# Kernel tuning notes

Hardware: AMD Instinct MI355X
Metric: run time of the kernel (lower is better)

## Reference

```python
import jax, jax.numpy as jnp
import numpy as np

BN_EPS = 1e-5


def setup_inputs() -> dict:
    key = jax.random.key(0)
    ks = jax.random.split(key, 6)
    B, C, K, N = 4, 64, 16, 16384  # batch, feat channels, neighbors, points
    W_OUT = 16  # weightnet output channels (fixed by Linear(16*mlp[-1], ...))
    xyz = jax.random.normal(ks[0], (B, N, 3), dtype=jnp.float32)
    points = jax.random.normal(ks[1], (B, C, K, N), dtype=jnp.float32)
    coordinate = jax.random.normal(ks[2], (B, 3, K, N), dtype=jnp.float32)
    w1 = jax.random.normal(ks[3], (W_OUT, 3), dtype=jnp.float32) * 0.5
    b1 = jnp.zeros((W_OUT,), dtype=jnp.float32)
    lin_w = jax.random.normal(ks[4], (C, W_OUT * C), dtype=jnp.float32) * (1.0 / np.sqrt(W_OUT * C))
    lin_b = jnp.zeros((C,), dtype=jnp.float32)
    gamma = jnp.ones((C,), dtype=jnp.float32)
    beta = jnp.zeros((C,), dtype=jnp.float32)
    return {"xyz": xyz, "points": points, "coordinate": coordinate,
            "w1": w1, "b1": b1, "lin_w": lin_w, "lin_b": lin_b,
            "gamma": gamma, "beta": beta}


def reference(xyz, points, coordinate, w1, b1, lin_w, lin_b, gamma, beta):
    B, C, K, N = points.shape
    # weightnet: 1x1 conv (3 -> 16) + ReLU over coordinate [B,3,K,N] -> [B,16,K,N]
    weights = jax.nn.relu(jnp.einsum('oc,bckn->bokn', w1, coordinate) + b1[None, :, None, None])
    # per-point aggregation: [B,N,C,K] @ [B,N,K,16] -> [B,N,C,16]
    new_points = jnp.einsum('bckn,bokn->bnco', points, weights)
    new_points = new_points.reshape(B, N, C * 16)  # [B, N, 16*C]
    # linear projection 16*C -> C
    new_points = jnp.einsum('bnk,ok->bno', new_points, lin_w) + lin_b  # [B, N, C]
    # BatchNorm1d over channel dim (training-mode batch stats), layout [B, C, N]
    new_points = new_points.transpose(0, 2, 1)  # [B, C, N]
    mean = jnp.mean(new_points, axis=(0, 2), keepdims=True)
    var = jnp.var(new_points, axis=(0, 2), keepdims=True)
    new_points = (new_points - mean) * jax.lax.rsqrt(var + BN_EPS)
    new_points = new_points * gamma[None, :, None] + beta[None, :, None]
    new_points = jax.nn.relu(new_points)  # [B, C, N]
    return (xyz, new_points)
```

## Files before the change

kernel.cpp:

```cpp
#include <hip/hip_runtime.h>

#define BB 4
#define CC 64
#define KK 16
#define NN 16384
#define NT 64
#define CH 8
#define NCH 8

typedef __attribute__((ext_vector_type(8))) short short8;
typedef __attribute__((ext_vector_type(4))) float floatx4;
typedef __attribute__((ext_vector_type(2))) _Float16 half2v;

__device__ __forceinline__ unsigned short f2bf_rtne(float x) {
    unsigned u = __builtin_bit_cast(unsigned, x);
    u += 0x7FFFu + ((u >> 16) & 1u);
    return (unsigned short)(u >> 16);
}

__device__ __forceinline__ unsigned pack_bf16x2(float lo, float hi) {
    unsigned a = __builtin_bit_cast(unsigned, lo) + 0x8000u;
    unsigned b = __builtin_bit_cast(unsigned, hi) + 0x8000u;
    return __builtin_amdgcn_perm(b, a, 0x07060302u);
}

__device__ __forceinline__ half2v cvt2h(float a, float b) {
    return __builtin_bit_cast(half2v, __builtin_amdgcn_cvt_pkrtz(a, b));
}

#if __has_builtin(__builtin_amdgcn_fdot2)
#define DOT2(a, b, c) __builtin_amdgcn_fdot2((a), (b), (c), false)
#else
__device__ __forceinline__ float dot2_fb(half2v a, half2v b, float c) {
    return fmaf((float)a[0], (float)b[0], fmaf((float)a[1], (float)b[1], c));
}
#define DOT2(a, b, c) dot2_fb((a), (b), (c))
#endif

__global__ __launch_bounds__(256)
void prep_bfrag(const float* __restrict__ lin_w, unsigned short* __restrict__ bfrag)
{
    const int tid  = blockIdx.x * 256 + threadIdx.x;
    const int lane = tid & 63;
    const int g    = tid >> 6;
    const int ci   = g >> 4;
    const int kk   = (g >> 2) & 3;
    const int nt   = g & 3;
    const int r    = lane & 15;
    const int sq   = lane >> 4;

    const float* src = lin_w + (size_t)(nt * 16 + r) * 1024 + ci * 128 + kk * 32 + sq * 8;
    unsigned short v[8];
    #pragma unroll
    for (int j = 0; j < 8; ++j) v[j] = f2bf_rtne(src[j]);
    *(uint4*)(bfrag + ((size_t)g * 64 + lane) * 8) = *(const uint4*)v;
}

__global__ __launch_bounds__(256, 4)
void fused_main(const float* __restrict__ points,
                const float* __restrict__ coordinate,
                const float* __restrict__ w1,
                const float* __restrict__ b1,
                const unsigned short* __restrict__ bfrag,
                float* __restrict__ y_out)
{
    __shared__ __align__(16) unsigned short s_a[NT][136];

    const int t    = threadIdx.x;
    const int lane = t & 63;
    const int q    = __builtin_amdgcn_readfirstlane(t >> 6);
    const int r    = lane & 15;
    const int sq   = lane >> 4;

    const int bid = blockIdx.x;
    const int b   = bid >> 8;
    const int n0  = (bid & 255) * NT;

    half2v wh[4][8];
    {
        const float* coordB = coordinate + (size_t)b * 3 * KK * NN + n0 + lane;
        float c0[KK], c1[KK], c2[KK];
        #pragma unroll
        for (int k = 0; k < KK; ++k) {
            c0[k] = coordB[(0 * KK + k) * NN];
            c1[k] = coordB[(1 * KK + k) * NN];
            c2[k] = coordB[(2 * KK + k) * NN];
        }
        #pragma unroll
        for (int j = 0; j < 4; ++j) {
            const int o = 4 * q + j;
            const float w1x = w1[o * 3 + 0];
            const float w1y = w1[o * 3 + 1];
            const float w1z = w1[o * 3 + 2];
            const float bo  = b1[o];
            #pragma unroll
            for (int kp = 0; kp < 8; ++kp) {
                float v0 = fmaf(w1x, c0[2 * kp],     fmaf(w1y, c1[2 * kp],     fmaf(w1z, c2[2 * kp],     bo)));
                float v1 = fmaf(w1x, c0[2 * kp + 1], fmaf(w1y, c1[2 * kp + 1], fmaf(w1z, c2[2 * kp + 1], bo)));
                wh[j][kp] = cvt2h(fmaxf(v0, 0.0f), fmaxf(v1, 0.0f));
            }
        }
    }

    floatx4 acc[4];
    #pragma unroll
    for (int nt = 0; nt < 4; ++nt) acc[nt] = (floatx4){0.f, 0.f, 0.f, 0.f};

    const float* pB = points + (size_t)b * CC * KK * NN + n0 + lane;

    for (int ci = 0; ci < NCH; ++ci) {
        uint2 packA[CH];
        #pragma unroll
        for (int cl = 0; cl < CH; ++cl) {
            const float* pc = pB + (size_t)(ci * CH + cl) * KK * NN;
            float pv[KK];
            #pragma unroll
            for (int k = 0; k < KK; ++k) pv[k] = pc[(size_t)k * NN];
            half2v ph[8];
            #pragma unroll
            for (int kp = 0; kp < 8; ++kp)
                ph[kp] = cvt2h(pv[2 * kp], pv[2 * kp + 1]);
            float a4[4];
            #pragma unroll
            for (int j = 0; j < 4; ++j) {
                float a = 0.f;
                #pragma unroll
                for (int kp = 0; kp < 8; ++kp) a = DOT2(ph[kp], wh[j][kp], a);
                a4[j] = a;
            }
            packA[cl].x = pack_bf16x2(a4[0], a4[1]);
            packA[cl].y = pack_bf16x2(a4[2], a4[3]);
        }

        __syncthreads();
        #pragma unroll
        for (int cl = 0; cl < CH; ++cl)
            *(uint2*)&s_a[lane][cl * 16 + 4 * q] = packA[cl];
        __syncthreads();

        #pragma unroll
        for (int kk = 0; kk < 4; ++kk) {
            const short8 af = *(const short8*)&s_a[16 * q + r][kk * 32 + sq * 8];
            #pragma unroll
            for (int nt = 0; nt < 4; ++nt) {
                const short8 bf = *(const short8*)
                    (bfrag + ((((size_t)ci * 4 + kk) * 4 + nt) * 64 + lane) * 8);
                acc[nt] = __builtin_amdgcn_mfma_f32_16x16x32_bf16(af, bf, acc[nt], 0, 0, 0);
            }
        }
    }

    float* yB = y_out + (size_t)b * CC * NN + n0;
    #pragma unroll
    for (int nt = 0; nt < 4; ++nt) {
        const int oc = nt * 16 + r;
        const float4 v = make_float4(acc[nt][0], acc[nt][1], acc[nt][2], acc[nt][3]);
        *(float4*)(yB + (size_t)oc * NN + 16 * q + 4 * sq) = v;
    }
}

__global__ __launch_bounds__(256)
void bn_reduce(const float* __restrict__ y, float* __restrict__ part)
{
    const int ch = blockIdx.x & 63;
    const int b  = blockIdx.x >> 6;
    const int t  = threadIdx.x;
    const float4* p = (const float4*)(y + ((size_t)b * CC + ch) * NN);
    float s = 0.f, ss = 0.f;
    for (int i = t; i < NN / 4; i += 256) {
        const float4 v = p[i];
        s  += v.x + v.y + v.z + v.w;
        ss += v.x * v.x + v.y * v.y + v.z * v.z + v.w * v.w;
    }
    #pragma unroll
    for (int m = 1; m < 64; m <<= 1) {
        s  += __shfl_xor(s, m);
        ss += __shfl_xor(ss, m);
    }
    __shared__ float rs[4], rss[4];
    if ((t & 63) == 0) { rs[t >> 6] = s; rss[t >> 6] = ss; }
    __syncthreads();
    if (t == 0) {
        part[blockIdx.x]       = rs[0] + rs[1] + rs[2] + rs[3];
        part[256 + blockIdx.x] = rss[0] + rss[1] + rss[2] + rss[3];
    }
}

__global__ void bn_stats(const float* __restrict__ part,
                         const float* __restrict__ gamma,
                         const float* __restrict__ beta,
                         float* __restrict__ ab)
{
    const int ch = threadIdx.x;
    float S = 0.f, SS = 0.f;
    #pragma unroll
    for (int b = 0; b < BB; ++b) {
        S  += part[b * 64 + ch];
        SS += part[256 + b * 64 + ch];
    }
    const float inv  = 1.0f / (float)(BB * NN);
    const float mean = S * inv;
    const float var  = SS * inv - mean * mean;
    const float a    = gamma[ch] * rsqrtf(var + 1e-5f);
    ab[ch]      = a;
    ab[CC + ch] = beta[ch] - mean * a;
}

__global__ __launch_bounds__(256)
void bn_apply(float* __restrict__ y, const float* __restrict__ ab)
{
    const size_t i = (size_t)blockIdx.x * 256 + threadIdx.x;
    float4* p = (float4*)y;
    float4 v = p[i];
    const int ch = (int)((i * 4) >> 14) & 63;
    const float a = ab[ch], bb = ab[CC + ch];
    v.x = fmaxf(fmaf(a, v.x, bb), 0.0f);
    v.y = fmaxf(fmaf(a, v.y, bb), 0.0f);
    v.z = fmaxf(fmaf(a, v.z, bb), 0.0f);
    v.w = fmaxf(fmaf(a, v.w, bb), 0.0f);
    p[i] = v;
}

extern "C" void kernel_launch(void* const* d_in, const int* in_sizes, int n_in,
                              void* d_out, int out_size, void* d_ws, size_t ws_size,
                              hipStream_t stream)
{
    const float* xyz        = (const float*)d_in[0];
    const float* points     = (const float*)d_in[1];
    const float* coordinate = (const float*)d_in[2];
    const float* w1         = (const float*)d_in[3];
    const float* b1         = (const float*)d_in[4];
    const float* lin_w      = (const float*)d_in[5];
    const float* gamma      = (const float*)d_in[7];
    const float* beta       = (const float*)d_in[8];

    float* out = (float*)d_out;

    unsigned short* bfrag = (unsigned short*)d_ws;
    float* part = (float*)d_ws + 32768;
    float* ab   = part + 512;

    const size_t xyz_elems = (size_t)BB * NN * 3;
    (void)hipMemcpyAsync(out, xyz, xyz_elems * sizeof(float),
                         hipMemcpyDeviceToDevice, stream);

    float* y_out = out + xyz_elems;

    prep_bfrag<<<32, 256, 0, stream>>>(lin_w, bfrag);
    fused_main<<<BB * (NN / NT), 256, 0, stream>>>(
        points, coordinate, w1, b1, bfrag, y_out);
    bn_reduce<<<BB * CC, 256, 0, stream>>>(y_out, part);
    bn_stats<<<1, 64, 0, stream>>>(part, gamma, beta, ab);
    bn_apply<<<(BB * CC * NN) / 4 / 256, 256, 0, stream>>>(y_out, ab);
}
```

Measured before the change: 458.7 us.

## Restructure fused kernel: 128-point blocks, software-prefetch points, double-buffered LDS

```diff
diff --git a/kernel.cpp b/kernel.cpp
--- a/kernel.cpp
+++ b/kernel.cpp
@@ -4,9 +4,7 @@
 #define CC 64
 #define KK 16
 #define NN 16384
-#define NT 64
-#define CH 8
-#define NCH 8
+#define NTB 128
 
 typedef __attribute__((ext_vector_type(8))) short short8;
 typedef __attribute__((ext_vector_type(4))) float floatx4;
@@ -56,7 +54,7 @@
     *(uint4*)(bfrag + ((size_t)g * 64 + lane) * 8) = *(const uint4*)v;
 }
 
-__global__ __launch_bounds__(256, 4)
+__global__ __launch_bounds__(256, 2)
 void fused_main(const float* __restrict__ points,
                 const float* __restrict__ coordinate,
                 const float* __restrict__ w1,
@@ -64,19 +62,21 @@
                 const unsigned short* __restrict__ bfrag,
                 float* __restrict__ y_out)
 {
-    __shared__ __align__(16) unsigned short s_a[NT][136];
+    __shared__ uint4 s_a[2][2][4 * 257];
 
     const int t    = threadIdx.x;
     const int lane = t & 63;
-    const int q    = __builtin_amdgcn_readfirstlane(t >> 6);
+    const int wv   = __builtin_amdgcn_readfirstlane(t >> 6);
+    const int P    = wv >> 1;
+    const int h    = wv & 1;
     const int r    = lane & 15;
     const int sq   = lane >> 4;
 
     const int bid = blockIdx.x;
-    const int b   = bid >> 8;
-    const int n0  = (bid & 255) * NT;
-
-    half2v wh[4][8];
+    const int b   = bid >> 7;
+    const int n0  = (bid & 127) * NTB + P * 64;
+
+    half2v wh[8][8];
     {
         const float* coordB = coordinate + (size_t)b * 3 * KK * NN + n0 + lane;
         float c0[KK], c1[KK], c2[KK];
@@ -87,8 +87,8 @@
             c2[k] = coordB[(2 * KK + k) * NN];
         }
         #pragma unroll
-        for (int j = 0; j < 4; ++j) {
-            const int o = 4 * q + j;
+        for (int j = 0; j < 8; ++j) {
+            const int o = 8 * h + j;
             const float w1x = w1[o * 3 + 0];
             const float w1y = w1[o * 3 + 1];
             const float w1z = w1[o * 3 + 2];
@@ -102,61 +102,95 @@
         }
     }
 
-    floatx4 acc[4];
-    #pragma unroll
-    for (int nt = 0; nt < 4; ++nt) acc[nt] = (floatx4){0.f, 0.f, 0.f, 0.f};
+    floatx4 acc[2][4];
+    #pragma unroll
+    for (int m = 0; m < 2; ++m)
+        #pragma unroll
+        for (int nt = 0; nt < 4; ++nt) acc[m][nt] = (floatx4){0.f, 0.f, 0.f, 0.f};
 
     const float* pB = points + (size_t)b * CC * KK * NN + n0 + lane;
 
-    for (int ci = 0; ci < NCH; ++ci) {
-        uint2 packA[CH];
-        #pragma unroll
-        for (int cl = 0; cl < CH; ++cl) {
-            const float* pc = pB + (size_t)(ci * CH + cl) * KK * NN;
-            float pv[KK];
-            #pragma unroll
-            for (int k = 0; k < KK; ++k) pv[k] = pc[(size_t)k * NN];
+    float pv[4][16];
+    #pragma unroll
+    for (int d = 0; d < 4; ++d)
+        #pragma unroll
+        for (int k = 0; k < KK; ++k)
+            pv[d][k] = pB[((size_t)d * KK + k) * NN];
+
+    for (int ci = 0; ci < 8; ++ci) {
+        const int buf = ci & 1;
+        uint4* saW = &s_a[P][buf][0];
+        #pragma unroll
+        for (int cl = 0; cl < 8; ++cl) {
+            const int cc   = ci * 8 + cl;
+            const int slot = cc & 3;
             half2v ph[8];
             #pragma unroll
             for (int kp = 0; kp < 8; ++kp)
-                ph[kp] = cvt2h(pv[2 * kp], pv[2 * kp + 1]);
-            float a4[4];
-            #pragma unroll
-            for (int j = 0; j < 4; ++j) {
+                ph[kp] = cvt2h(pv[slot][2 * kp], pv[slot][2 * kp + 1]);
+            {
+                const int cp = (cc + 4 < CC) ? (cc + 4) : (CC - 1);
+                #pragma unroll
+                for (int k = 0; k < KK; ++k)
+                    pv[slot][k] = pB[((size_t)cp * KK + k) * NN];
+            }
+            float a8[8];
+            #pragma unroll
+            for (int j = 0; j < 8; ++j) {
                 float a = 0.f;
                 #pragma unroll
                 for (int kp = 0; kp < 8; ++kp) a = DOT2(ph[kp], wh[j][kp], a);
-                a4[j] = a;
-            }
-            packA[cl].x = pack_bf16x2(a4[0], a4[1]);
-            packA[cl].y = pack_bf16x2(a4[2], a4[3]);
-        }
-
-        __syncthreads();
-        #pragma unroll
-        for (int cl = 0; cl < CH; ++cl)
-            *(uint2*)&s_a[lane][cl * 16 + 4 * q] = packA[cl];
-        __syncthreads();
-
+                a8[j] = a;
+            }
+            uint4 pk;
+            pk.x = pack_bf16x2(a8[0], a8[1]);
+            pk.y = pack_bf16x2(a8[2], a8[3]);
+            pk.z = pack_bf16x2(a8[4], a8[5]);
+            pk.w = pack_bf16x2(a8[6], a8[7]);
+            saW[(lane >> 4) * 257 + (cl >> 1) * 64 + (lane & 15) * 4 + (cl & 1) * 2 + h] = pk;
+        }
+
+        uint4 bf_c[4];
+        #pragma unroll
+        for (int nt = 0; nt < 4; ++nt)
+            bf_c[nt] = *(const uint4*)(bfrag + ((((size_t)ci * 4 + 0) * 4 + nt) * 64 + lane) * 8);
+
+        asm volatile("s_waitcnt lgkmcnt(0)\n\ts_barrier" ::: "memory");
+
+        const uint4* saR = &s_a[P][buf][0];
         #pragma unroll
         for (int kk = 0; kk < 4; ++kk) {
-            const short8 af = *(const short8*)&s_a[16 * q + r][kk * 32 + sq * 8];
-            #pragma unroll
-            for (int nt = 0; nt < 4; ++nt) {
-                const short8 bf = *(const short8*)
-                    (bfrag + ((((size_t)ci * 4 + kk) * 4 + nt) * 64 + lane) * 8);
-                acc[nt] = __builtin_amdgcn_mfma_f32_16x16x32_bf16(af, bf, acc[nt], 0, 0, 0);
-            }
+            uint4 bf_n[4];
+            if (kk < 3) {
+                #pragma unroll
+                for (int nt = 0; nt < 4; ++nt)
+                    bf_n[nt] = *(const uint4*)(bfrag + ((((size_t)ci * 4 + kk + 1) * 4 + nt) * 64 + lane) * 8);
+            }
+            short8 af[2];
+            #pragma unroll
+            for (int m = 0; m < 2; ++m)
+                af[m] = __builtin_bit_cast(short8, saR[(2 * h + m) * 257 + kk * 64 + r * 4 + sq]);
+            #pragma unroll
+            for (int m = 0; m < 2; ++m)
+                #pragma unroll
+                for (int nt = 0; nt < 4; ++nt)
+                    acc[m][nt] = __builtin_amdgcn_mfma_f32_16x16x32_bf16(
+                        af[m], __builtin_bit_cast(short8, bf_c[nt]), acc[m][nt], 0, 0, 0);
+            #pragma unroll
+            for (int nt = 0; nt < 4; ++nt) bf_c[nt] = bf_n[nt];
         }
     }
 
     float* yB = y_out + (size_t)b * CC * NN + n0;
     #pragma unroll
-    for (int nt = 0; nt < 4; ++nt) {
-        const int oc = nt * 16 + r;
-        const float4 v = make_float4(acc[nt][0], acc[nt][1], acc[nt][2], acc[nt][3]);
-        *(float4*)(yB + (size_t)oc * NN + 16 * q + 4 * sq) = v;
-    }
+    for (int m = 0; m < 2; ++m)
+        #pragma unroll
+        for (int nt = 0; nt < 4; ++nt) {
+            const int oc = nt * 16 + r;
+            const float4 v = make_float4(acc[m][nt][0], acc[m][nt][1],
+                                         acc[m][nt][2], acc[m][nt][3]);
+            *(float4*)(yB + (size_t)oc * NN + (2 * h + m) * 16 + sq * 4) = v;
+        }
 }
 
 __global__ __launch_bounds__(256)
@@ -247,7 +281,7 @@
     float* y_out = out + xyz_elems;
 
     prep_bfrag<<<32, 256, 0, stream>>>(lin_w, bfrag);
-    fused_main<<<BB * (NN / NT), 256, 0, stream>>>(
+    fused_main<<<BB * (NN / NTB), 256, 0, stream>>>(
         points, coordinate, w1, b1, bfrag, y_out);
     bn_reduce<<<BB * CC, 256, 0, stream>>>(y_out, part);
     bn_stats<<<1, 64, 0, stream>>>(part, gamma, beta, ab);
```

Result: faster. 407.5 us (-11.1%).
